# Kernel tuning notes

Measured on AMD Instinct MI355X. Metric: run time of the kernel, lower is better.

Reference implementation:

```python
import jax, jax.numpy as jnp
import numpy as np

N_VOX, N_COLS = 200000, 5   # (N, 1 + 3 coords + 1 feat)
N_CLUSTS, PTS_PER_CLUST = 1024, 128
N_EDGES = 8192


def setup_inputs() -> dict:
    key = jax.random.key(0)
    k1, k2, k3 = jax.random.split(key, 3)
    data = jax.random.normal(k1, (N_VOX, N_COLS), dtype=jnp.float32)
    clusts = jax.random.randint(k2, (N_CLUSTS, PTS_PER_CLUST), 0, N_VOX)
    edge_index = jax.random.randint(k3, (2, N_EDGES), 0, N_CLUSTS)
    return {"data": data, "clusts": clusts, "edge_index": edge_index}


def reference(data, clusts, edge_index):
    # COORD_COLS = columns 1:4 of the sparse tensor
    voxels = data[:, 1:4]                       # [N, 3]
    pts = voxels[clusts]                        # [C, P, 3]
    x1 = pts[edge_index[0]]                     # [E, P, 3] first cluster of each edge
    x2 = pts[edge_index[1]]                     # [E, P, 3] second cluster
    P = x1.shape[1]

    # per-edge pairwise squared distances (argmin of d^2 == argmin of d)
    d2 = jnp.sum((x1[:, :, None, :] - x2[:, None, :, :]) ** 2, axis=-1)  # [E, P, P]
    imin = jnp.argmin(d2.reshape(d2.shape[0], -1), axis=1)               # [E]
    i1, i2 = imin // P, imin % P

    v1 = jnp.take_along_axis(x1, i1[:, None, None], axis=1)[:, 0, :]     # [E, 3]
    v2 = jnp.take_along_axis(x2, i2[:, None, None], axis=1)[:, 0, :]     # [E, 3]

    disp = v1 - v2
    lend = jnp.linalg.norm(disp, axis=-1, keepdims=True)                 # [E, 1]
    safe = jnp.where(lend > 0, lend, 1.0)
    dispn = jnp.where(lend > 0, disp / safe, disp)                       # unit displacement

    B = (dispn[:, :, None] * dispn[:, None, :]).reshape(-1, 9)           # outer product, [E, 9]

    feats = jnp.concatenate([v1, v2, dispn, lend, B], axis=1)            # [E, 19]
    # undirected: interleave original and flipped (v1<->v2, disp -> -disp, B invariant)
    feats_flip = jnp.concatenate([v2, v1, -dispn, lend, B], axis=1)
    full = jnp.stack([feats, feats_flip], axis=1).reshape(-1, 19)        # [2E, 19]
    return full
```

## Files before the change

### kernel.cpp

```cpp
#include <hip/hip_runtime.h>
#include <cstdint>

#define NV 200000
#define NCOLS 5
#define P 128
#define NE 8192
#define NC 1024

__global__ __launch_bounds__(256) void gather_kernel(
    const float* __restrict__ data,
    const int*   __restrict__ clusts,
    float4*      __restrict__ ws)
{
    const int idx = blockIdx.x * 256 + threadIdx.x;
    const int v = clusts[idx];
    ws[idx] = make_float4(data[v * NCOLS + 1], data[v * NCOLS + 2],
                          data[v * NCOLS + 3], 0.f);
}

template <bool USE_WS>
__global__ __launch_bounds__(128) void clust_geo_edge_kernel(
    const float*  __restrict__ data,
    const int*    __restrict__ clusts,
    const int*    __restrict__ edge_index,
    const float4* __restrict__ ws,
    float*        __restrict__ out)
{
    const int w    = threadIdx.x >> 6;
    const int lane = threadIdx.x & 63;
    const int e    = blockIdx.x * 2 + w;

    __shared__ float4 x1s[2][P];
    __shared__ float4 x2s[2][P];

    const int c1 = edge_index[e];
    const int c2 = edge_index[NE + e];

    if (USE_WS) {
        x1s[w][lane]      = ws[c1 * P + lane];
        x1s[w][lane + 64] = ws[c1 * P + lane + 64];
        x2s[w][lane]      = ws[c2 * P + lane];
        x2s[w][lane + 64] = ws[c2 * P + lane + 64];
    } else {
        int v = clusts[c1 * P + lane];
        x1s[w][lane]      = make_float4(data[v * NCOLS + 1], data[v * NCOLS + 2],
                                        data[v * NCOLS + 3], 0.f);
        v = clusts[c1 * P + lane + 64];
        x1s[w][lane + 64] = make_float4(data[v * NCOLS + 1], data[v * NCOLS + 2],
                                        data[v * NCOLS + 3], 0.f);
        v = clusts[c2 * P + lane];
        x2s[w][lane]      = make_float4(data[v * NCOLS + 1], data[v * NCOLS + 2],
                                        data[v * NCOLS + 3], 0.f);
        v = clusts[c2 * P + lane + 64];
        x2s[w][lane + 64] = make_float4(data[v * NCOLS + 1], data[v * NCOLS + 2],
                                        data[v * NCOLS + 3], 0.f);
    }

    const int tj = lane & 15;
    const int ti = lane >> 4;

    float bx[8], by[8], bz[8];
    #pragma unroll
    for (int m = 0; m < 8; ++m) {
        const float4 v = x2s[w][tj + 16 * m];
        bx[m] = v.x; by[m] = v.y; bz[m] = v.z;
    }

    float bd[8];
    int   bk[8];
    #pragma unroll
    for (int m = 0; m < 8; ++m) { bd[m] = __builtin_inff(); bk[m] = 0; }

    #pragma unroll 1
    for (int kk = 0; kk < 8; ++kk) {
        float ax[4], ay[4], az[4];
        #pragma unroll
        for (int u = 0; u < 4; ++u) {
            const float4 av = x1s[w][ti + 4 * (kk * 4 + u)];
            ax[u] = av.x; ay[u] = av.y; az[u] = av.z;
        }
        #pragma unroll
        for (int u = 0; u < 4; ++u) {
            #pragma unroll
            for (int m = 0; m < 8; ++m) {
                const float dx = __fsub_rn(ax[u], bx[m]);
                const float dy = __fsub_rn(ay[u], by[m]);
                const float dz = __fsub_rn(az[u], bz[m]);
                const float d2 = __fadd_rn(__fadd_rn(__fmul_rn(dx, dx), __fmul_rn(dy, dy)),
                                           __fmul_rn(dz, dz));
                if (d2 < bd[m]) { bd[m] = d2; bk[m] = kk * 4 + u; }
            }
        }
    }

    const int base = ti * P + tj;
    unsigned long long key = 0xffffffffffffffffull;
    #pragma unroll
    for (int m = 0; m < 8; ++m) {
        const unsigned flat = (unsigned)(base + (m << 4) + (bk[m] << 9));
        const unsigned long long km =
            ((unsigned long long)__float_as_uint(bd[m]) << 32) | flat;
        if (km < key) key = km;
    }

    for (int off = 32; off > 0; off >>= 1) {
        unsigned long long other = __shfl_down(key, off, 64);
        if (other < key) key = other;
    }

    if (lane == 0) {
        const int flat = (int)(key & 0xffffffffull);
        const int i1 = flat >> 7;
        const int i2 = flat & (P - 1);

        const float v1x = x1s[w][i1].x, v1y = x1s[w][i1].y, v1z = x1s[w][i1].z;
        const float v2x = x2s[w][i2].x, v2y = x2s[w][i2].y, v2z = x2s[w][i2].z;

        const float dx = v1x - v2x, dy = v1y - v2y, dz = v1z - v2z;
        const float lend = sqrtf(dx * dx + dy * dy + dz * dz);

        float nx, ny, nz;
        if (lend > 0.f) { nx = dx / lend; ny = dy / lend; nz = dz / lend; }
        else            { nx = dx;        ny = dy;        nz = dz;        }

        const float B0 = nx * nx, B1 = nx * ny, B2 = nx * nz;
        const float B3 = ny * nx, B4 = ny * ny, B5 = ny * nz;
        const float B6 = nz * nx, B7 = nz * ny, B8 = nz * nz;

        float2* o = reinterpret_cast<float2*>(out + (size_t)e * 38);
        o[0]  = make_float2(v1x, v1y);
        o[1]  = make_float2(v1z, v2x);
        o[2]  = make_float2(v2y, v2z);
        o[3]  = make_float2(nx,  ny);
        o[4]  = make_float2(nz,  lend);
        o[5]  = make_float2(B0,  B1);
        o[6]  = make_float2(B2,  B3);
        o[7]  = make_float2(B4,  B5);
        o[8]  = make_float2(B6,  B7);
        o[9]  = make_float2(B8,  v2x);
        o[10] = make_float2(v2y, v2z);
        o[11] = make_float2(v1x, v1y);
        o[12] = make_float2(v1z, -nx);
        o[13] = make_float2(-ny, -nz);
        o[14] = make_float2(lend, B0);
        o[15] = make_float2(B1,  B2);
        o[16] = make_float2(B3,  B4);
        o[17] = make_float2(B5,  B6);
        o[18] = make_float2(B7,  B8);
    }
}

extern "C" void kernel_launch(void* const* d_in, const int* in_sizes, int n_in,
                              void* d_out, int out_size, void* d_ws, size_t ws_size,
                              hipStream_t stream) {
    const float* data       = (const float*)d_in[0];
    const int*   clusts     = (const int*)d_in[1];
    const int*   edge_index = (const int*)d_in[2];
    float*       out        = (float*)d_out;
    float4*      ws         = (float4*)d_ws;

    const size_t need = (size_t)NC * P * sizeof(float4);
    if (ws_size >= need) {
        gather_kernel<<<(NC * P) / 256, 256, 0, stream>>>(data, clusts, ws);
        clust_geo_edge_kernel<true><<<NE / 2, 128, 0, stream>>>(data, clusts, edge_index, ws, out);
    } else {
        clust_geo_edge_kernel<false><<<NE / 2, 128, 0, stream>>>(data, clusts, edge_index, ws, out);
    }
}
```

Measured before the change: 95.34 us.

## Process two edges per wave with prefetch, register-loaded B points, no x2 LDS

Each wave now handles two edges, prefetching the second edge's x1 points and x2 points while computing the first. The x2 points go straight from global memory into registers, so there is no shared-memory staging for them, and the epilogue reloads only the chosen x2 point. The inner loop unroll goes from 4 to 8 x1 points per iteration, and the grid is halved. This aims to hide load latency and cut LDS traffic, at the cost of higher register pressure, fewer blocks, and redundant global loads across lanes for the B points.

```diff
diff --git a/kernel.cpp b/kernel.cpp
--- a/kernel.cpp
+++ b/kernel.cpp
@@ -16,6 +16,116 @@
     const int v = clusts[idx];
     ws[idx] = make_float4(data[v * NCOLS + 1], data[v * NCOLS + 2],
                           data[v * NCOLS + 3], 0.f);
+}
+
+template <bool USE_WS>
+__device__ __forceinline__ float4 load_pt(const float* __restrict__ data,
+                                          const int*   __restrict__ clusts,
+                                          const float4* __restrict__ ws,
+                                          int c, int p)
+{
+    if (USE_WS) return ws[c * P + p];
+    const int v = clusts[c * P + p];
+    return make_float4(data[v * NCOLS + 1], data[v * NCOLS + 2],
+                       data[v * NCOLS + 3], 0.f);
+}
+
+__device__ __forceinline__ unsigned long long
+wave_min_key(const float4* __restrict__ x1p,
+             const float* __restrict__ bx, const float* __restrict__ by,
+             const float* __restrict__ bz, int ti, int tj)
+{
+    float bd[8];
+    int   bk[8];
+    #pragma unroll
+    for (int m = 0; m < 8; ++m) { bd[m] = __builtin_inff(); bk[m] = 0; }
+
+    #pragma unroll 1
+    for (int kk = 0; kk < 4; ++kk) {
+        float ax[8], ay[8], az[8];
+        #pragma unroll
+        for (int u = 0; u < 8; ++u) {
+            const float4 av = x1p[ti + 4 * (kk * 8 + u)];
+            ax[u] = av.x; ay[u] = av.y; az[u] = av.z;
+        }
+        #pragma unroll
+        for (int u = 0; u < 8; ++u) {
+            #pragma unroll
+            for (int m = 0; m < 8; ++m) {
+                const float dx = __fsub_rn(ax[u], bx[m]);
+                const float dy = __fsub_rn(ay[u], by[m]);
+                const float dz = __fsub_rn(az[u], bz[m]);
+                const float d2 = __fadd_rn(__fadd_rn(__fmul_rn(dx, dx), __fmul_rn(dy, dy)),
+                                           __fmul_rn(dz, dz));
+                if (d2 < bd[m]) { bd[m] = d2; bk[m] = kk * 8 + u; }
+            }
+        }
+    }
+
+    const int base = ti * P + tj;
+    unsigned long long key = 0xffffffffffffffffull;
+    #pragma unroll
+    for (int m = 0; m < 8; ++m) {
+        const unsigned flat = (unsigned)(base + (m << 4) + (bk[m] << 9));
+        const unsigned long long km =
+            ((unsigned long long)__float_as_uint(bd[m]) << 32) | flat;
+        if (km < key) key = km;
+    }
+
+    for (int off = 32; off > 0; off >>= 1) {
+        unsigned long long other = __shfl_down(key, off, 64);
+        if (other < key) key = other;
+    }
+    return key;
+}
+
+template <bool USE_WS>
+__device__ __forceinline__ void epilogue(
+    unsigned long long key, const float4* __restrict__ x1p,
+    const float* __restrict__ data, const int* __restrict__ clusts,
+    const float4* __restrict__ ws, int c2, int e,
+    float* __restrict__ out)
+{
+    const int flat = (int)(key & 0xffffffffull);
+    const int i1 = flat >> 7;
+    const int i2 = flat & (P - 1);
+
+    const float4 p1 = x1p[i1];
+    const float4 p2 = load_pt<USE_WS>(data, clusts, ws, c2, i2);
+    const float v1x = p1.x, v1y = p1.y, v1z = p1.z;
+    const float v2x = p2.x, v2y = p2.y, v2z = p2.z;
+
+    const float dx = v1x - v2x, dy = v1y - v2y, dz = v1z - v2z;
+    const float lend = sqrtf(dx * dx + dy * dy + dz * dz);
+
+    float nx, ny, nz;
+    if (lend > 0.f) { nx = dx / lend; ny = dy / lend; nz = dz / lend; }
+    else            { nx = dx;        ny = dy;        nz = dz;        }
+
+    const float B0 = nx * nx, B1 = nx * ny, B2 = nx * nz;
+    const float B3 = ny * nx, B4 = ny * ny, B5 = ny * nz;
+    const float B6 = nz * nx, B7 = nz * ny, B8 = nz * nz;
+
+    float2* o = reinterpret_cast<float2*>(out + (size_t)e * 38);
+    o[0]  = make_float2(v1x, v1y);
+    o[1]  = make_float2(v1z, v2x);
+    o[2]  = make_float2(v2y, v2z);
+    o[3]  = make_float2(nx,  ny);
+    o[4]  = make_float2(nz,  lend);
+    o[5]  = make_float2(B0,  B1);
+    o[6]  = make_float2(B2,  B3);
+    o[7]  = make_float2(B4,  B5);
+    o[8]  = make_float2(B6,  B7);
+    o[9]  = make_float2(B8,  v2x);
+    o[10] = make_float2(v2y, v2z);
+    o[11] = make_float2(v1x, v1y);
+    o[12] = make_float2(v1z, -nx);
+    o[13] = make_float2(-ny, -nz);
+    o[14] = make_float2(lend, B0);
+    o[15] = make_float2(B1,  B2);
+    o[16] = make_float2(B3,  B4);
+    o[17] = make_float2(B5,  B6);
+    o[18] = make_float2(B7,  B8);
 }
 
 template <bool USE_WS>
@@ -26,128 +136,61 @@
     const float4* __restrict__ ws,
     float*        __restrict__ out)
 {
+#pragma clang fp contract(off)
     const int w    = threadIdx.x >> 6;
     const int lane = threadIdx.x & 63;
-    const int e    = blockIdx.x * 2 + w;
-
-    __shared__ float4 x1s[2][P];
-    __shared__ float4 x2s[2][P];
-
-    const int c1 = edge_index[e];
-    const int c2 = edge_index[NE + e];
-
-    if (USE_WS) {
-        x1s[w][lane]      = ws[c1 * P + lane];
-        x1s[w][lane + 64] = ws[c1 * P + lane + 64];
-        x2s[w][lane]      = ws[c2 * P + lane];
-        x2s[w][lane + 64] = ws[c2 * P + lane + 64];
-    } else {
-        int v = clusts[c1 * P + lane];
-        x1s[w][lane]      = make_float4(data[v * NCOLS + 1], data[v * NCOLS + 2],
-                                        data[v * NCOLS + 3], 0.f);
-        v = clusts[c1 * P + lane + 64];
-        x1s[w][lane + 64] = make_float4(data[v * NCOLS + 1], data[v * NCOLS + 2],
-                                        data[v * NCOLS + 3], 0.f);
-        v = clusts[c2 * P + lane];
-        x2s[w][lane]      = make_float4(data[v * NCOLS + 1], data[v * NCOLS + 2],
-                                        data[v * NCOLS + 3], 0.f);
-        v = clusts[c2 * P + lane + 64];
-        x2s[w][lane + 64] = make_float4(data[v * NCOLS + 1], data[v * NCOLS + 2],
-                                        data[v * NCOLS + 3], 0.f);
-    }
+    const int W    = blockIdx.x * 2 + w;
+
+    __shared__ float4 x1buf[2][2][P];
 
     const int tj = lane & 15;
     const int ti = lane >> 4;
 
+    const int e0   = W;
+    const int c1_0 = edge_index[e0];
+    const int c2_0 = edge_index[NE + e0];
+    const int e1   = W + NE / 2;
+    const int c1_1 = edge_index[e1];
+    const int c2_1 = edge_index[NE + e1];
+
+    const float4 A0  = load_pt<USE_WS>(data, clusts, ws, c1_0, lane);
+    const float4 A1  = load_pt<USE_WS>(data, clusts, ws, c1_0, lane + 64);
+    float4 Bv[8];
+    #pragma unroll
+    for (int m = 0; m < 8; ++m)
+        Bv[m] = load_pt<USE_WS>(data, clusts, ws, c2_0, tj + 16 * m);
+    const float4 A0n = load_pt<USE_WS>(data, clusts, ws, c1_1, lane);
+    const float4 A1n = load_pt<USE_WS>(data, clusts, ws, c1_1, lane + 64);
+
+    const float4* x1p0 = &x1buf[w][0][0];
+    x1buf[w][0][lane]      = A0;
+    x1buf[w][0][lane + 64] = A1;
+
     float bx[8], by[8], bz[8];
     #pragma unroll
-    for (int m = 0; m < 8; ++m) {
-        const float4 v = x2s[w][tj + 16 * m];
-        bx[m] = v.x; by[m] = v.y; bz[m] = v.z;
-    }
-
-    float bd[8];
-    int   bk[8];
-    #pragma unroll
-    for (int m = 0; m < 8; ++m) { bd[m] = __builtin_inff(); bk[m] = 0; }
-
-    #pragma unroll 1
-    for (int kk = 0; kk < 8; ++kk) {
-        float ax[4], ay[4], az[4];
-        #pragma unroll
-        for (int u = 0; u < 4; ++u) {
-            const float4 av = x1s[w][ti + 4 * (kk * 4 + u)];
-            ax[u] = av.x; ay[u] = av.y; az[u] = av.z;
-        }
-        #pragma unroll
-        for (int u = 0; u < 4; ++u) {
-            #pragma unroll
-            for (int m = 0; m < 8; ++m) {
-                const float dx = __fsub_rn(ax[u], bx[m]);
-                const float dy = __fsub_rn(ay[u], by[m]);
-                const float dz = __fsub_rn(az[u], bz[m]);
-                const float d2 = __fadd_rn(__fadd_rn(__fmul_rn(dx, dx), __fmul_rn(dy, dy)),
-                                           __fmul_rn(dz, dz));
-                if (d2 < bd[m]) { bd[m] = d2; bk[m] = kk * 4 + u; }
-            }
-        }
-    }
-
-    const int base = ti * P + tj;
-    unsigned long long key = 0xffffffffffffffffull;
-    #pragma unroll
-    for (int m = 0; m < 8; ++m) {
-        const unsigned flat = (unsigned)(base + (m << 4) + (bk[m] << 9));
-        const unsigned long long km =
-            ((unsigned long long)__float_as_uint(bd[m]) << 32) | flat;
-        if (km < key) key = km;
-    }
-
-    for (int off = 32; off > 0; off >>= 1) {
-        unsigned long long other = __shfl_down(key, off, 64);
-        if (other < key) key = other;
-    }
-
-    if (lane == 0) {
-        const int flat = (int)(key & 0xffffffffull);
-        const int i1 = flat >> 7;
-        const int i2 = flat & (P - 1);
-
-        const float v1x = x1s[w][i1].x, v1y = x1s[w][i1].y, v1z = x1s[w][i1].z;
-        const float v2x = x2s[w][i2].x, v2y = x2s[w][i2].y, v2z = x2s[w][i2].z;
-
-        const float dx = v1x - v2x, dy = v1y - v2y, dz = v1z - v2z;
-        const float lend = sqrtf(dx * dx + dy * dy + dz * dz);
-
-        float nx, ny, nz;
-        if (lend > 0.f) { nx = dx / lend; ny = dy / lend; nz = dz / lend; }
-        else            { nx = dx;        ny = dy;        nz = dz;        }
-
-        const float B0 = nx * nx, B1 = nx * ny, B2 = nx * nz;
-        const float B3 = ny * nx, B4 = ny * ny, B5 = ny * nz;
-        const float B6 = nz * nx, B7 = nz * ny, B8 = nz * nz;
-
-        float2* o = reinterpret_cast<float2*>(out + (size_t)e * 38);
-        o[0]  = make_float2(v1x, v1y);
-        o[1]  = make_float2(v1z, v2x);
-        o[2]  = make_float2(v2y, v2z);
-        o[3]  = make_float2(nx,  ny);
-        o[4]  = make_float2(nz,  lend);
-        o[5]  = make_float2(B0,  B1);
-        o[6]  = make_float2(B2,  B3);
-        o[7]  = make_float2(B4,  B5);
-        o[8]  = make_float2(B6,  B7);
-        o[9]  = make_float2(B8,  v2x);
-        o[10] = make_float2(v2y, v2z);
-        o[11] = make_float2(v1x, v1y);
-        o[12] = make_float2(v1z, -nx);
-        o[13] = make_float2(-ny, -nz);
-        o[14] = make_float2(lend, B0);
-        o[15] = make_float2(B1,  B2);
-        o[16] = make_float2(B3,  B4);
-        o[17] = make_float2(B5,  B6);
-        o[18] = make_float2(B7,  B8);
-    }
+    for (int m = 0; m < 8; ++m) { bx[m] = Bv[m].x; by[m] = Bv[m].y; bz[m] = Bv[m].z; }
+
+    const unsigned long long key0 = wave_min_key(x1p0, bx, by, bz, ti, tj);
+
+    const float4* x1p1 = &x1buf[w][1][0];
+    x1buf[w][1][lane]      = A0n;
+    x1buf[w][1][lane + 64] = A1n;
+
+    float4 Bn[8];
+    #pragma unroll
+    for (int m = 0; m < 8; ++m)
+        Bn[m] = load_pt<USE_WS>(data, clusts, ws, c2_1, tj + 16 * m);
+
+    if (lane == 0)
+        epilogue<USE_WS>(key0, x1p0, data, clusts, ws, c2_0, e0, out);
+
+    #pragma unroll
+    for (int m = 0; m < 8; ++m) { bx[m] = Bn[m].x; by[m] = Bn[m].y; bz[m] = Bn[m].z; }
+
+    const unsigned long long key1 = wave_min_key(x1p1, bx, by, bz, ti, tj);
+
+    if (lane == 0)
+        epilogue<USE_WS>(key1, x1p1, data, clusts, ws, c2_1, e1, out);
 }
 
 extern "C" void kernel_launch(void* const* d_in, const int* in_sizes, int n_in,
@@ -162,8 +205,8 @@
     const size_t need = (size_t)NC * P * sizeof(float4);
     if (ws_size >= need) {
         gather_kernel<<<(NC * P) / 256, 256, 0, stream>>>(data, clusts, ws);
-        clust_geo_edge_kernel<true><<<NE / 2, 128, 0, stream>>>(data, clusts, edge_index, ws, out);
+        clust_geo_edge_kernel<true><<<NE / 4, 128, 0, stream>>>(data, clusts, edge_index, ws, out);
     } else {
-        clust_geo_edge_kernel<false><<<NE / 2, 128, 0, stream>>>(data, clusts, edge_index, ws, out);
-    }
-}
+        clust_geo_edge_kernel<false><<<NE / 4, 128, 0, stream>>>(data, clusts, edge_index, ws, out);
+    }
+}
```

After: 95.96 us. Within noise of the previous version (+0.7%).
